# Performance work log

Hardware: AMD Instinct MI355X
Metric: run time of the kernel (lower is better)

The kernel has to match this reference:

```python
import jax, jax.numpy as jnp
import numpy as np

B, T, D = 2, 2048, 1024
H = 16
DK = D // H


def setup_inputs() -> dict:
    key = jax.random.key(0)
    ks = jax.random.split(key, 5)
    s = 1.0 / np.sqrt(D)
    return {
        "x": jax.random.normal(ks[0], (B, T, D), dtype=jnp.float32),
        "Wq": jax.random.normal(ks[1], (D, D), dtype=jnp.float32) * s,
        "bq": jnp.zeros((D,), dtype=jnp.float32),
        "Wk": jax.random.normal(ks[2], (D, D), dtype=jnp.float32) * s,
        "bk": jnp.zeros((D,), dtype=jnp.float32),
        "Wv": jax.random.normal(ks[3], (D, D), dtype=jnp.float32) * s,
        "bv": jnp.zeros((D,), dtype=jnp.float32),
        "Wo": jax.random.normal(ks[4], (D, D), dtype=jnp.float32) * s,
        "bo": jnp.zeros((D,), dtype=jnp.float32),
    }


def reference(x, Wq, bq, Wk, bk, Wv, bv, Wo, bo):
    # projections (torch Linear: x @ W.T + b; here W is stored as (in, out))
    Q = x @ Wq + bq  # (B,T,D)
    K = x @ Wk + bk
    V = x @ Wv + bv
    # split heads -> (B,H,T,dk)
    Q = Q.reshape(B, T, H, DK).transpose(0, 2, 1, 3)
    K = K.reshape(B, T, H, DK).transpose(0, 2, 1, 3)
    V = V.reshape(B, T, H, DK).transpose(0, 2, 1, 3)
    scale = 1.0 / jnp.sqrt(jnp.asarray(DK, dtype=x.dtype))
    scores = jnp.einsum("bhqd,bhkd->bhqk", Q, K) * scale  # (B,H,T,T)
    causal = jnp.tril(jnp.ones((T, T), dtype=bool))
    scores = jnp.where(causal, scores, -jnp.inf)
    weights = jax.nn.softmax(scores, axis=-1)
    # dropout is identity in eval mode
    context = jnp.einsum("bhqk,bhkd->bhqd", weights, V)
    context = context.transpose(0, 2, 1, 3).reshape(B, T, D)
    return context @ Wo + bo
```

## Files before the change

kernel.cpp:

```cpp
#include <hip/hip_runtime.h>
#include <hip/hip_bf16.h>

constexpr int Bc = 2;
constexpr int Tc = 2048;
constexpr int Mc = Bc * Tc;
constexpr float CfQ = 0.18033688011112042f;

typedef __attribute__((ext_vector_type(8))) __bf16 bf16x8;
typedef __attribute__((ext_vector_type(4))) __bf16 bf16x4;
typedef __attribute__((ext_vector_type(4))) float floatx4;

__device__ __forceinline__ void gl_lds16(const void* g, void* l) {
    __builtin_amdgcn_global_load_lds(
        (const __attribute__((address_space(1))) void*)g,
        (__attribute__((address_space(3))) void*)l, 16, 0, 0);
}

__global__ __launch_bounds__(256) void prep_all(const float* __restrict__ x,
                                                const float* __restrict__ Wq,
                                                const float* __restrict__ Wk,
                                                const float* __restrict__ Wv,
                                                const float* __restrict__ Wo,
                                                __bf16* __restrict__ xb,
                                                __bf16* __restrict__ Wqkv,
                                                __bf16* __restrict__ Wot) {
    const int z = blockIdx.z;
    const int tid = threadIdx.x;
    if (z >= 4) {
        const int lb = blockIdx.y * 16 + blockIdx.x;
        const size_t base = ((size_t)(z - 4) * 256 + lb) * 4096;
#pragma unroll
        for (int it = 0; it < 4; ++it) {
            const size_t i = base + (size_t)(it * 256 + tid) * 4;
            const float4 v = *(const float4*)(x + i);
            bf16x4 r;
            r[0] = (__bf16)v.x; r[1] = (__bf16)v.y;
            r[2] = (__bf16)v.z; r[3] = (__bf16)v.w;
            *(bf16x4*)(xb + i) = r;
        }
        return;
    }
    __shared__ float t[64][65];
    const float* W = (z == 0) ? Wq : (z == 1) ? Wk : (z == 2) ? Wv : Wo;
    __bf16* Wt = (z < 3) ? Wqkv + (size_t)z * 1024 * 1024 : Wot;
    const int k0 = blockIdx.y * 64, n0 = blockIdx.x * 64;
    const int c = tid & 63, r0 = tid >> 6;
#pragma unroll
    for (int i = 0; i < 16; ++i)
        t[r0 + i * 4][c] = W[(size_t)(k0 + r0 + i * 4) * 1024 + n0 + c];
    __syncthreads();
#pragma unroll
    for (int i = 0; i < 16; ++i) {
        const int r = r0 + i * 4;
        Wt[(size_t)(n0 + r) * 1024 + k0 + c] = (__bf16)t[c][r];
    }
}

template <int TN, bool BF16_OUT, bool FUSE_VT>
__global__ __launch_bounds__(256) void gemm_bt(const __bf16* __restrict__ A,
                                               const __bf16* __restrict__ Bt,
                                               const float* __restrict__ b0,
                                               const float* __restrict__ b1,
                                               const float* __restrict__ b2,
                                               void* __restrict__ Cv,
                                               __bf16* __restrict__ Vt,
                                               int K, int ldc) {
    constexpr int NI = TN / 32;
    __shared__ __bf16 As[128 * 64];
    __shared__ __bf16 Bs[TN * 64];
    const int tid = threadIdx.x, lane = tid & 63, wave = tid >> 6;
    const int wm = wave & 1, wn = wave >> 1;
    const int bm = blockIdx.y * 128, bn = blockIdx.x * TN;
    const __bf16* Ab = A + (size_t)bm * K;
    const __bf16* Bb = Bt + (size_t)bn * K;
    const int quad = lane >> 4, tm = lane & 15;
    const int tsw = tm & 7;

    floatx4 acc[4][NI] = {};

    for (int k0 = 0; k0 < K; k0 += 64) {
#pragma unroll
        for (int i = 0; i < 4; ++i) {
            const int s = i * 256 + tid;
            const int row = s >> 3;
            const int lc = (s & 7) ^ (row & 7);
            gl_lds16(Ab + (size_t)row * K + k0 + lc * 8, As + s * 8);
        }
#pragma unroll
        for (int i = 0; i < TN / 32; ++i) {
            const int s = i * 256 + tid;
            const int row = s >> 3;
            const int lc = (s & 7) ^ (row & 7);
            gl_lds16(Bb + (size_t)row * K + k0 + lc * 8, Bs + s * 8);
        }
        __syncthreads();
        bf16x8 af[4][2], bfv[NI][2];
#pragma unroll
        for (int mi = 0; mi < 4; ++mi) {
            const int row = (wm * 64 + mi * 16 + tm) * 64;
#pragma unroll
            for (int ks = 0; ks < 2; ++ks)
                af[mi][ks] = *(const bf16x8*)(As + row + ((ks * 4 + quad) ^ tsw) * 8);
        }
#pragma unroll
        for (int ni = 0; ni < NI; ++ni) {
            const int row = (wn * (TN / 2) + ni * 16 + tm) * 64;
#pragma unroll
            for (int ks = 0; ks < 2; ++ks)
                bfv[ni][ks] = *(const bf16x8*)(Bs + row + ((ks * 4 + quad) ^ tsw) * 8);
        }
#pragma unroll
        for (int ks = 0; ks < 2; ++ks)
#pragma unroll
            for (int mi = 0; mi < 4; ++mi)
#pragma unroll
                for (int ni = 0; ni < NI; ++ni)
                    acc[mi][ni] = __builtin_amdgcn_mfma_f32_16x16x32_bf16(
                        af[mi][ks], bfv[ni][ks], acc[mi][ni], 0, 0, 0);
        __syncthreads();
    }

#pragma unroll
    for (int ni = 0; ni < NI; ++ni) {
        const int gc = bn + wn * (TN / 2) + ni * 16 + tm;
        const float bias = (gc < 1024) ? b0[gc]
                         : (gc < 2048) ? b1[gc - 1024]
                                       : b2[gc - 2048];
        const float scale = (FUSE_VT && gc < 1024) ? CfQ : 1.0f;
#pragma unroll
        for (int mi = 0; mi < 4; ++mi) {
            const int gr0 = bm + wm * 64 + mi * 16 + quad * 4;
            if (FUSE_VT && gc >= 2048) {
                bf16x4 pv;
#pragma unroll
                for (int r = 0; r < 4; ++r) pv[r] = (__bf16)(acc[mi][ni][r] + bias);
                const int bb = gr0 >> 11, tloc = gr0 & 2047;
                const int hh = (gc - 2048) >> 6, dd = gc & 63;
                const int tperm = (tloc & ~63) + ((tloc >> 2) & 3) * 16 +
                                  ((tloc >> 4) & 3) * 4;
                *(bf16x4*)(Vt + ((size_t)(bb * 16 + hh) * 64 + dd) * 2048 + tperm) = pv;
            } else if (BF16_OUT) {
#pragma unroll
                for (int r = 0; r < 4; ++r)
                    ((__bf16*)Cv)[(size_t)(gr0 + r) * ldc + gc] =
                        (__bf16)((acc[mi][ni][r] + bias) * scale);
            } else {
#pragma unroll
                for (int r = 0; r < 4; ++r)
                    ((float*)Cv)[(size_t)(gr0 + r) * ldc + gc] =
                        acc[mi][ni][r] + bias;
            }
        }
    }
}

__global__ __launch_bounds__(512, 4) void attn_mfma(const __bf16* __restrict__ QK,
                                                    const __bf16* __restrict__ Vt,
                                                    __bf16* __restrict__ ctx) {
    constexpr float NEG = -1e30f;

    __shared__ __bf16 Ks[2][2][64 * 64];
    __shared__ __bf16 Vts[2][2][64 * 64];

    const int tid = threadIdx.x, lane = tid & 63, w = tid >> 6;
    const int g = w >> 2, wq = w & 3;
    const int c = lane & 15, quad = lane >> 4;
    const int n = blockIdx.x;
    const int bh = (n & 7) * 4 + ((n >> 3) & 3);
    const int ip = n >> 5;
    const int b = bh >> 4, h = bh & 15;

    const __bf16* Qb = QK + (size_t)(b * Tc) * 2048 + h * 64;
    const __bf16* Kb = Qb + 1024;
    const __bf16* Vtb = Vt + (size_t)bh * 64 * 2048;

    const int sw = c & 7;
    int koff0[4], koff1[4];
#pragma unroll
    for (int ni = 0; ni < 4; ++ni) {
        const int krow = ni * 16 + c;
        koff0[ni] = krow * 64 + (quad ^ sw) * 8;
        koff1[ni] = krow * 64 + ((4 + quad) ^ sw) * 8;
    }
    int voff[4][2];
#pragma unroll
    for (int di = 0; di < 4; ++di) {
        const int vrow = di * 16 + c;
#pragma unroll
        for (int pr = 0; pr < 2; ++pr)
            voff[di][pr] = vrow * 64 + ((quad * 2 + pr) ^ sw) * 8;
    }

    const int srow = tid >> 3;
    const int slc = (tid & 7) ^ (srow & 7);
    const __bf16* kgB = Kb + (size_t)srow * 2048 + slc * 8;
    const __bf16* vgB = Vtb + (size_t)srow * 2048 + slc * 8;

#pragma unroll 1
    for (int ph = 0; ph < 2; ++ph) {
        const int qt = ph ? 31 - ip : ip;
        const int nk = qt + 1;
        const int npair = (nk + 1) >> 1;

        const __bf16* qr = Qb + (size_t)(qt * 64 + wq * 16 + c) * 2048;
        const bf16x8 qf0 = *(const bf16x8*)(qr + quad * 8);
        const bf16x8 qf1 = *(const bf16x8*)(qr + 32 + quad * 8);

        floatx4 lacc = {};
        floatx4 oa[4] = {};

        auto stage = [&](int p, int sbuf) {
            const __bf16* kg = kgB + (size_t)(2 * p) * 64 * 2048;
            const __bf16* vg = vgB + 2 * p * 64;
            __bf16* kd = &Ks[sbuf][0][tid * 8];
            __bf16* vd = &Vts[sbuf][0][tid * 8];
            gl_lds16(kg, kd);
            gl_lds16(kg + (size_t)64 * 2048, kd + 4096);
            gl_lds16(vg, vd);
            gl_lds16(vg + 64, vd + 4096);
        };

        stage(0, 0);
        if (npair > 1) stage(1, 1);

        for (int kp = 0; kp < npair; ++kp) {
            const int buf = kp & 1;
            if (kp + 1 < npair) {
                asm volatile("s_waitcnt vmcnt(4)" ::: "memory");
            } else {
                asm volatile("s_waitcnt vmcnt(0)" ::: "memory");
            }
            __builtin_amdgcn_sched_barrier(0);
            __builtin_amdgcn_s_barrier();

            const int kt = 2 * kp + g;
            if (kt < nk) {
                const __bf16* ks = Ks[buf][g];
                const __bf16* vs = Vts[buf][g];

                float sv[4][4];
                __builtin_amdgcn_s_setprio(1);
#pragma unroll
                for (int ni = 0; ni < 4; ++ni) {
                    const bf16x8 kb0 = *(const bf16x8*)(ks + koff0[ni]);
                    const bf16x8 kb1 = *(const bf16x8*)(ks + koff1[ni]);
                    floatx4 a = {};
                    a = __builtin_amdgcn_mfma_f32_16x16x32_bf16(kb0, qf0, a, 0, 0, 0);
                    a = __builtin_amdgcn_mfma_f32_16x16x32_bf16(kb1, qf1, a, 0, 0, 0);
#pragma unroll
                    for (int r = 0; r < 4; ++r) sv[ni][r] = a[r];
                }
                __builtin_amdgcn_s_setprio(0);

                if (kt == qt) {
#pragma unroll
                    for (int ni = 0; ni < 4; ++ni)
#pragma unroll
                        for (int r = 0; r < 4; ++r)
                            if (ni * 16 + quad * 4 + r > wq * 16 + c) sv[ni][r] = NEG;
                }
#pragma unroll
                for (int ni = 0; ni < 4; ++ni) {
#pragma unroll
                    for (int r = 0; r < 4; ++r) sv[ni][r] = __builtin_exp2f(sv[ni][r]);
                    lacc[0] += sv[ni][0];
                    lacc[1] += sv[ni][1];
                    lacc[2] += sv[ni][2];
                    lacc[3] += sv[ni][3];
                }

                bf16x8 pb[2];
#pragma unroll
                for (int pr = 0; pr < 2; ++pr)
#pragma unroll
                    for (int j = 0; j < 4; ++j) {
                        pb[pr][j] = (__bf16)sv[pr * 2][j];
                        pb[pr][4 + j] = (__bf16)sv[pr * 2 + 1][j];
                    }

                __builtin_amdgcn_s_setprio(1);
#pragma unroll
                for (int di = 0; di < 4; ++di) {
#pragma unroll
                    for (int pr = 0; pr < 2; ++pr) {
                        const bf16x8 vf = *(const bf16x8*)(vs + voff[di][pr]);
                        oa[di] = __builtin_amdgcn_mfma_f32_16x16x32_bf16(
                            vf, pb[pr], oa[di], 0, 0, 0);
                    }
                }
                __builtin_amdgcn_s_setprio(0);
            }
            __builtin_amdgcn_sched_barrier(0);
            __builtin_amdgcn_s_barrier();
            if (kp + 2 < npair) stage(kp + 2, buf);
        }

        __syncthreads();
        float lsum = lacc[0] + lacc[1] + lacc[2] + lacc[3];
        float* sc = (float*)&Ks[0][0][0];
        if (g == 1) {
#pragma unroll
            for (int di = 0; di < 4; ++di)
                *(floatx4*)(sc + wq * 1088 + di * 256 + lane * 4) = oa[di];
            sc[wq * 1088 + 1024 + lane] = lsum;
        }
        __syncthreads();
        if (g == 0) {
#pragma unroll
            for (int di = 0; di < 4; ++di)
                oa[di] += *(const floatx4*)(sc + wq * 1088 + di * 256 + lane * 4);
            lsum += sc[wq * 1088 + 1024 + lane];
            lsum += __shfl_xor(lsum, 16);
            lsum += __shfl_xor(lsum, 32);
            const float inv = 1.f / lsum;
            __bf16* cp = ctx + (size_t)(b * Tc + qt * 64 + wq * 16 + c) * 1024 +
                         h * 64 + quad * 4;
#pragma unroll
            for (int di = 0; di < 4; ++di) {
                bf16x4 rv;
#pragma unroll
                for (int r = 0; r < 4; ++r) rv[r] = (__bf16)(oa[di][r] * inv);
                *(bf16x4*)(cp + di * 16) = rv;
            }
        }
        __syncthreads();
    }
}

extern "C" void kernel_launch(void* const* d_in, const int* in_sizes, int n_in,
                              void* d_out, int out_size, void* d_ws, size_t ws_size,
                              hipStream_t stream) {
    const float* x  = (const float*)d_in[0];
    const float* Wq = (const float*)d_in[1];
    const float* bq = (const float*)d_in[2];
    const float* Wk = (const float*)d_in[3];
    const float* bk = (const float*)d_in[4];
    const float* Wv = (const float*)d_in[5];
    const float* bv = (const float*)d_in[6];
    const float* Wo = (const float*)d_in[7];
    const float* bo = (const float*)d_in[8];

    __bf16* xb   = (__bf16*)d_ws;
    __bf16* Wqkv = xb + (size_t)Mc * 1024;
    __bf16* Wot  = Wqkv + (size_t)3072 * 1024;
    __bf16* QKb  = Wot + (size_t)1024 * 1024;
    __bf16* Vtw  = QKb + (size_t)Mc * 2048;
    __bf16* ctxb = xb;

    prep_all<<<dim3(16, 16, 8), 256, 0, stream>>>(x, Wq, Wk, Wv, Wo,
                                                  xb, Wqkv, Wot);

    gemm_bt<128, true, true><<<dim3(24, 32), 256, 0, stream>>>(
        xb, Wqkv, bq, bk, bv, QKb, Vtw, 1024, 2048);

    attn_mfma<<<dim3(512), 512, 0, stream>>>(QKb, Vtw, ctxb);

    gemm_bt<64, false, false><<<dim3(16, 32), 256, 0, stream>>>(
        ctxb, Wot, bo, bo, bo, d_out, nullptr, 1024, 1024);
}
```

Before: 179.8 us.

## Switch attention to 32x32x16 MFMA with 128-row query tiles

Rewrites the attention kernel to use 32x32x16 bf16 MFMA instead of 16x16x32. Each block now covers 128 query rows (32 per wave), so the grid halves to 256 blocks. The probability fragments are repacked through cross-lane shuffles so they can feed the PV MFMA directly, which removes the V^T time permutation in the projection GEMM epilogue. Larger tiles reuse K/V in shared memory more and issue fewer MFMA instructions, but the kernel holds more registers (launch bounds relaxed to 2 waves per SIMD) and has fewer blocks to balance the causal work.

```diff
diff --git a/kernel.cpp b/kernel.cpp
--- a/kernel.cpp
+++ b/kernel.cpp
@@ -9,11 +9,19 @@
 typedef __attribute__((ext_vector_type(8))) __bf16 bf16x8;
 typedef __attribute__((ext_vector_type(4))) __bf16 bf16x4;
 typedef __attribute__((ext_vector_type(4))) float floatx4;
+typedef __attribute__((ext_vector_type(16))) float f32x16;
+typedef __attribute__((ext_vector_type(4))) unsigned int uint4v;
 
 __device__ __forceinline__ void gl_lds16(const void* g, void* l) {
     __builtin_amdgcn_global_load_lds(
         (const __attribute__((address_space(1))) void*)g,
         (__attribute__((address_space(3))) void*)l, 16, 0, 0);
+}
+
+__device__ __forceinline__ unsigned int pkbf(float x, float y) {
+    union { __bf16 h[2]; unsigned int u; } z;
+    z.h[0] = (__bf16)x; z.h[1] = (__bf16)y;
+    return z.u;
 }
 
 __global__ __launch_bounds__(256) void prep_all(const float* __restrict__ x,
@@ -136,9 +144,7 @@
                 for (int r = 0; r < 4; ++r) pv[r] = (__bf16)(acc[mi][ni][r] + bias);
                 const int bb = gr0 >> 11, tloc = gr0 & 2047;
                 const int hh = (gc - 2048) >> 6, dd = gc & 63;
-                const int tperm = (tloc & ~63) + ((tloc >> 2) & 3) * 16 +
-                                  ((tloc >> 4) & 3) * 4;
-                *(bf16x4*)(Vt + ((size_t)(bb * 16 + hh) * 64 + dd) * 2048 + tperm) = pv;
+                *(bf16x4*)(Vt + ((size_t)(bb * 16 + hh) * 64 + dd) * 2048 + tloc) = pv;
             } else if (BF16_OUT) {
 #pragma unroll
                 for (int r = 0; r < 4; ++r)
@@ -154,7 +160,7 @@
     }
 }
 
-__global__ __launch_bounds__(512, 4) void attn_mfma(const __bf16* __restrict__ QK,
+__global__ __launch_bounds__(512, 2) void attn_mfma(const __bf16* __restrict__ QK,
                                                     const __bf16* __restrict__ Vt,
                                                     __bf16* __restrict__ ctx) {
     constexpr float NEG = -1e30f;
@@ -163,8 +169,8 @@
     __shared__ __bf16 Vts[2][2][64 * 64];
 
     const int tid = threadIdx.x, lane = tid & 63, w = tid >> 6;
-    const int g = w >> 2, wq = w & 3;
-    const int c = lane & 15, quad = lane >> 4;
+    const int g = w >> 2, ws = w & 3;
+    const int col = lane & 31, hi = lane >> 5;
     const int n = blockIdx.x;
     const int bh = (n & 7) * 4 + ((n >> 3) & 3);
     const int ip = n >> 5;
@@ -174,22 +180,13 @@
     const __bf16* Kb = Qb + 1024;
     const __bf16* Vtb = Vt + (size_t)bh * 64 * 2048;
 
-    const int sw = c & 7;
-    int koff0[4], koff1[4];
-#pragma unroll
-    for (int ni = 0; ni < 4; ++ni) {
-        const int krow = ni * 16 + c;
-        koff0[ni] = krow * 64 + (quad ^ sw) * 8;
-        koff1[ni] = krow * 64 + ((4 + quad) ^ sw) * 8;
-    }
-    int voff[4][2];
-#pragma unroll
-    for (int di = 0; di < 4; ++di) {
-        const int vrow = di * 16 + c;
-#pragma unroll
-        for (int pr = 0; pr < 2; ++pr)
-            voff[di][pr] = vrow * 64 + ((quad * 2 + pr) ^ sw) * 8;
-    }
+    const int sw = col & 7;
+    int off[2][4];
+#pragma unroll
+    for (int i = 0; i < 2; ++i)
+#pragma unroll
+        for (int cc = 0; cc < 4; ++cc)
+            off[i][cc] = (i * 32 + col) * 64 + (((cc * 2 + hi) ^ sw) * 8);
 
     const int srow = tid >> 3;
     const int slc = (tid & 7) ^ (srow & 7);
@@ -198,16 +195,18 @@
 
 #pragma unroll 1
     for (int ph = 0; ph < 2; ++ph) {
-        const int qt = ph ? 31 - ip : ip;
-        const int nk = qt + 1;
-        const int npair = (nk + 1) >> 1;
-
-        const __bf16* qr = Qb + (size_t)(qt * 64 + wq * 16 + c) * 2048;
-        const bf16x8 qf0 = *(const bf16x8*)(qr + quad * 8);
-        const bf16x8 qf1 = *(const bf16x8*)(qr + 32 + quad * 8);
+        const int qt = ph ? 15 - ip : ip;
+        const int npair = qt + 1;
+        const int qbase = qt * 128 + ws * 32;
+
+        const __bf16* qr = Qb + (size_t)(qbase + col) * 2048;
+        bf16x8 qf[4];
+#pragma unroll
+        for (int dkc = 0; dkc < 4; ++dkc)
+            qf[dkc] = *(const bf16x8*)(qr + dkc * 16 + hi * 8);
 
         floatx4 lacc = {};
-        floatx4 oa[4] = {};
+        f32x16 oa[2] = {};
 
         auto stage = [&](int p, int sbuf) {
             const __bf16* kg = kgB + (size_t)(2 * p) * 64 * 2048;
@@ -234,60 +233,67 @@
             __builtin_amdgcn_s_barrier();
 
             const int kt = 2 * kp + g;
-            if (kt < nk) {
+            const int kbase = kt * 64;
+            if (kbase <= qbase + 31) {
                 const __bf16* ks = Ks[buf][g];
                 const __bf16* vs = Vts[buf][g];
 
-                float sv[4][4];
+                f32x16 acc[2] = {};
                 __builtin_amdgcn_s_setprio(1);
 #pragma unroll
-                for (int ni = 0; ni < 4; ++ni) {
-                    const bf16x8 kb0 = *(const bf16x8*)(ks + koff0[ni]);
-                    const bf16x8 kb1 = *(const bf16x8*)(ks + koff1[ni]);
-                    floatx4 a = {};
-                    a = __builtin_amdgcn_mfma_f32_16x16x32_bf16(kb0, qf0, a, 0, 0, 0);
-                    a = __builtin_amdgcn_mfma_f32_16x16x32_bf16(kb1, qf1, a, 0, 0, 0);
-#pragma unroll
-                    for (int r = 0; r < 4; ++r) sv[ni][r] = a[r];
-                }
+                for (int kt2 = 0; kt2 < 2; ++kt2)
+#pragma unroll
+                    for (int dkc = 0; dkc < 4; ++dkc) {
+                        const bf16x8 kb = *(const bf16x8*)(ks + off[kt2][dkc]);
+                        acc[kt2] = __builtin_amdgcn_mfma_f32_32x32x16_bf16(
+                            kb, qf[dkc], acc[kt2], 0, 0, 0);
+                    }
                 __builtin_amdgcn_s_setprio(0);
 
-                if (kt == qt) {
-#pragma unroll
-                    for (int ni = 0; ni < 4; ++ni)
-#pragma unroll
-                        for (int r = 0; r < 4; ++r)
-                            if (ni * 16 + quad * 4 + r > wq * 16 + c) sv[ni][r] = NEG;
-                }
-#pragma unroll
-                for (int ni = 0; ni < 4; ++ni) {
-#pragma unroll
-                    for (int r = 0; r < 4; ++r) sv[ni][r] = __builtin_exp2f(sv[ni][r]);
-                    lacc[0] += sv[ni][0];
-                    lacc[1] += sv[ni][1];
-                    lacc[2] += sv[ni][2];
-                    lacc[3] += sv[ni][3];
-                }
-
-                bf16x8 pb[2];
-#pragma unroll
-                for (int pr = 0; pr < 2; ++pr)
-#pragma unroll
-                    for (int j = 0; j < 4; ++j) {
-                        pb[pr][j] = (__bf16)sv[pr * 2][j];
-                        pb[pr][4 + j] = (__bf16)sv[pr * 2 + 1][j];
+                if (kp == npair - 1) {
+#pragma unroll
+                    for (int kt2 = 0; kt2 < 2; ++kt2)
+#pragma unroll
+                        for (int reg = 0; reg < 16; ++reg) {
+                            const int kloc = kt2 * 32 + (reg & 3) + 8 * (reg >> 2) + 4 * hi;
+                            if (kbase + kloc > qbase + col) acc[kt2][reg] = NEG;
+                        }
+                }
+#pragma unroll
+                for (int kt2 = 0; kt2 < 2; ++kt2)
+#pragma unroll
+                    for (int reg = 0; reg < 16; ++reg) {
+                        const float p = __builtin_exp2f(acc[kt2][reg]);
+                        acc[kt2][reg] = p;
+                        lacc[reg & 3] += p;
                     }
 
+                bf16x8 pf[4];
+#pragma unroll
+                for (int tc = 0; tc < 4; ++tc) {
+                    const int kt2 = tc >> 1, c16 = (tc & 1) * 8;
+                    const unsigned int a0 = pkbf(acc[kt2][c16 + 0], acc[kt2][c16 + 1]);
+                    const unsigned int a1 = pkbf(acc[kt2][c16 + 2], acc[kt2][c16 + 3]);
+                    const unsigned int b0 = pkbf(acc[kt2][c16 + 4], acc[kt2][c16 + 5]);
+                    const unsigned int b1 = pkbf(acc[kt2][c16 + 6], acc[kt2][c16 + 7]);
+                    const unsigned int s0 = hi ? a0 : b0, s1 = hi ? a1 : b1;
+                    const unsigned int r0 = __shfl_xor(s0, 32);
+                    const unsigned int r1 = __shfl_xor(s1, 32);
+                    uint4v dv;
+                    dv[0] = hi ? r0 : a0; dv[1] = hi ? r1 : a1;
+                    dv[2] = hi ? b0 : r0; dv[3] = hi ? b1 : r1;
+                    pf[tc] = __builtin_bit_cast(bf16x8, dv);
+                }
+
                 __builtin_amdgcn_s_setprio(1);
 #pragma unroll
-                for (int di = 0; di < 4; ++di) {
-#pragma unroll
-                    for (int pr = 0; pr < 2; ++pr) {
-                        const bf16x8 vf = *(const bf16x8*)(vs + voff[di][pr]);
-                        oa[di] = __builtin_amdgcn_mfma_f32_16x16x32_bf16(
-                            vf, pb[pr], oa[di], 0, 0, 0);
+                for (int dt = 0; dt < 2; ++dt)
+#pragma unroll
+                    for (int tc = 0; tc < 4; ++tc) {
+                        const bf16x8 vf = *(const bf16x8*)(vs + off[dt][tc]);
+                        oa[dt] = __builtin_amdgcn_mfma_f32_32x32x16_bf16(
+                            vf, pf[tc], oa[dt], 0, 0, 0);
                     }
-                }
                 __builtin_amdgcn_s_setprio(0);
             }
             __builtin_amdgcn_sched_barrier(0);
@@ -296,32 +302,46 @@
         }
 
         __syncthreads();
-        float lsum = lacc[0] + lacc[1] + lacc[2] + lacc[3];
-        float* sc = (float*)&Ks[0][0][0];
+        float lt = lacc[0] + lacc[1] + lacc[2] + lacc[3];
+        lt += __shfl_xor(lt, 32);
+        float* sco = (float*)&Ks[0][0][0];
+        float* scl = (float*)&Vts[0][0][0];
         if (g == 1) {
 #pragma unroll
-            for (int di = 0; di < 4; ++di)
-                *(floatx4*)(sc + wq * 1088 + di * 256 + lane * 4) = oa[di];
-            sc[wq * 1088 + 1024 + lane] = lsum;
+            for (int dt = 0; dt < 2; ++dt)
+#pragma unroll
+                for (int a = 0; a < 4; ++a) {
+                    floatx4 t4;
+                    t4[0] = oa[dt][4 * a + 0]; t4[1] = oa[dt][4 * a + 1];
+                    t4[2] = oa[dt][4 * a + 2]; t4[3] = oa[dt][4 * a + 3];
+                    *(floatx4*)(sco + (dt * 4 + a) * 1024 + ws * 256 + lane * 4) = t4;
+                }
+            scl[ws * 64 + lane] = lt;
         }
         __syncthreads();
         if (g == 0) {
 #pragma unroll
-            for (int di = 0; di < 4; ++di)
-                oa[di] += *(const floatx4*)(sc + wq * 1088 + di * 256 + lane * 4);
-            lsum += sc[wq * 1088 + 1024 + lane];
-            lsum += __shfl_xor(lsum, 16);
-            lsum += __shfl_xor(lsum, 32);
-            const float inv = 1.f / lsum;
-            __bf16* cp = ctx + (size_t)(b * Tc + qt * 64 + wq * 16 + c) * 1024 +
-                         h * 64 + quad * 4;
-#pragma unroll
-            for (int di = 0; di < 4; ++di) {
-                bf16x4 rv;
-#pragma unroll
-                for (int r = 0; r < 4; ++r) rv[r] = (__bf16)(oa[di][r] * inv);
-                *(bf16x4*)(cp + di * 16) = rv;
-            }
+            for (int dt = 0; dt < 2; ++dt)
+#pragma unroll
+                for (int a = 0; a < 4; ++a) {
+                    const floatx4 t4 =
+                        *(const floatx4*)(sco + (dt * 4 + a) * 1024 + ws * 256 + lane * 4);
+                    oa[dt][4 * a + 0] += t4[0]; oa[dt][4 * a + 1] += t4[1];
+                    oa[dt][4 * a + 2] += t4[2]; oa[dt][4 * a + 3] += t4[3];
+                }
+            lt += scl[ws * 64 + lane];
+            const float inv = 1.f / lt;
+            __bf16* cp = ctx + (size_t)(b * Tc + qbase + col) * 1024 + h * 64 + hi * 4;
+#pragma unroll
+            for (int dt = 0; dt < 2; ++dt)
+#pragma unroll
+                for (int a = 0; a < 4; ++a) {
+                    bf16x4 rv;
+#pragma unroll
+                    for (int r = 0; r < 4; ++r)
+                        rv[r] = (__bf16)(oa[dt][4 * a + r] * inv);
+                    *(bf16x4*)(cp + dt * 32 + a * 8) = rv;
+                }
         }
         __syncthreads();
     }
@@ -353,7 +373,7 @@
     gemm_bt<128, true, true><<<dim3(24, 32), 256, 0, stream>>>(
         xb, Wqkv, bq, bk, bv, QKb, Vtw, 1024, 2048);
 
-    attn_mfma<<<dim3(512), 512, 0, stream>>>(QKb, Vtw, ctxb);
+    attn_mfma<<<dim3(256), 512, 0, stream>>>(QKb, Vtw, ctxb);
 
     gemm_bt<64, false, false><<<dim3(16, 32), 256, 0, stream>>>(
         ctxb, Wot, bo, bo, bo, d_out, nullptr, 1024, 1024);
```

New measurement: 193.1 us. 7.4% more time.

## Double-buffer GEMM LDS tiles with K=32 steps and async prefetch

Applied to the files above, without the earlier changes.

Restructures the bf16 GEMM main loop into a two-stage software pipeline. K-step shrinks from 64 to 32, LDS tiles are double-buffered, and direct global-to-LDS loads for step k+2 are issued while step k computes. Manual vmcnt waits and s_setprio around the MFMA block replace the per-iteration load/sync/compute serialization, with the XOR swizzle adjusted for 32-wide rows. The risks are that hand-counted vmcnt values are fragile, and that the smaller K-step means twice as many barriers.

```diff
diff --git a/kernel.cpp b/kernel.cpp
--- a/kernel.cpp
+++ b/kernel.cpp
@@ -66,58 +66,73 @@
                                                __bf16* __restrict__ Vt,
                                                int K, int ldc) {
     constexpr int NI = TN / 32;
-    __shared__ __bf16 As[128 * 64];
-    __shared__ __bf16 Bs[TN * 64];
+    constexpr int NB = TN / 64;
+    __shared__ __bf16 As[2][128 * 32];
+    __shared__ __bf16 Bs[2][TN * 32];
     const int tid = threadIdx.x, lane = tid & 63, wave = tid >> 6;
     const int wm = wave & 1, wn = wave >> 1;
     const int bm = blockIdx.y * 128, bn = blockIdx.x * TN;
     const __bf16* Ab = A + (size_t)bm * K;
     const __bf16* Bb = Bt + (size_t)bn * K;
     const int quad = lane >> 4, tm = lane & 15;
-    const int tsw = tm & 7;
+    const int xsw = (tm >> 1) & 3;
 
     floatx4 acc[4][NI] = {};
 
-    for (int k0 = 0; k0 < K; k0 += 64) {
-#pragma unroll
-        for (int i = 0; i < 4; ++i) {
+    auto stage = [&](int k0, int sbuf) {
+#pragma unroll
+        for (int i = 0; i < 2; ++i) {
             const int s = i * 256 + tid;
-            const int row = s >> 3;
-            const int lc = (s & 7) ^ (row & 7);
-            gl_lds16(Ab + (size_t)row * K + k0 + lc * 8, As + s * 8);
-        }
-#pragma unroll
-        for (int i = 0; i < TN / 32; ++i) {
+            const int row = s >> 2;
+            const int lc = (s & 3) ^ ((row >> 1) & 3);
+            gl_lds16(Ab + (size_t)row * K + k0 + lc * 8, &As[sbuf][s * 8]);
+        }
+#pragma unroll
+        for (int i = 0; i < NB; ++i) {
             const int s = i * 256 + tid;
-            const int row = s >> 3;
-            const int lc = (s & 7) ^ (row & 7);
-            gl_lds16(Bb + (size_t)row * K + k0 + lc * 8, Bs + s * 8);
-        }
-        __syncthreads();
-        bf16x8 af[4][2], bfv[NI][2];
-#pragma unroll
-        for (int mi = 0; mi < 4; ++mi) {
-            const int row = (wm * 64 + mi * 16 + tm) * 64;
-#pragma unroll
-            for (int ks = 0; ks < 2; ++ks)
-                af[mi][ks] = *(const bf16x8*)(As + row + ((ks * 4 + quad) ^ tsw) * 8);
-        }
-#pragma unroll
-        for (int ni = 0; ni < NI; ++ni) {
-            const int row = (wn * (TN / 2) + ni * 16 + tm) * 64;
-#pragma unroll
-            for (int ks = 0; ks < 2; ++ks)
-                bfv[ni][ks] = *(const bf16x8*)(Bs + row + ((ks * 4 + quad) ^ tsw) * 8);
-        }
-#pragma unroll
-        for (int ks = 0; ks < 2; ++ks)
-#pragma unroll
-            for (int mi = 0; mi < 4; ++mi)
-#pragma unroll
-                for (int ni = 0; ni < NI; ++ni)
-                    acc[mi][ni] = __builtin_amdgcn_mfma_f32_16x16x32_bf16(
-                        af[mi][ks], bfv[ni][ks], acc[mi][ni], 0, 0, 0);
-        __syncthreads();
+            const int row = s >> 2;
+            const int lc = (s & 3) ^ ((row >> 1) & 3);
+            gl_lds16(Bb + (size_t)row * K + k0 + lc * 8, &Bs[sbuf][s * 8]);
+        }
+    };
+
+    const int nstep = K >> 5;
+    stage(0, 0);
+    stage(32, 1);
+
+    for (int ks = 0; ks < nstep; ++ks) {
+        const int buf = ks & 1;
+        if (ks + 1 < nstep) {
+            if constexpr (TN == 128)
+                asm volatile("s_waitcnt vmcnt(4)" ::: "memory");
+            else
+                asm volatile("s_waitcnt vmcnt(3)" ::: "memory");
+        } else {
+            asm volatile("s_waitcnt vmcnt(0)" ::: "memory");
+        }
+        __builtin_amdgcn_sched_barrier(0);
+        __builtin_amdgcn_s_barrier();
+
+        bf16x8 af[4], bfv[NI];
+#pragma unroll
+        for (int mi = 0; mi < 4; ++mi)
+            af[mi] = *(const bf16x8*)(&As[buf][(wm * 64 + mi * 16 + tm) * 32 +
+                                               ((quad ^ xsw) * 8)]);
+#pragma unroll
+        for (int ni = 0; ni < NI; ++ni)
+            bfv[ni] = *(const bf16x8*)(&Bs[buf][(wn * (TN / 2) + ni * 16 + tm) * 32 +
+                                                ((quad ^ xsw) * 8)]);
+        __builtin_amdgcn_s_setprio(1);
+#pragma unroll
+        for (int mi = 0; mi < 4; ++mi)
+#pragma unroll
+            for (int ni = 0; ni < NI; ++ni)
+                acc[mi][ni] = __builtin_amdgcn_mfma_f32_16x16x32_bf16(
+                    af[mi], bfv[ni], acc[mi][ni], 0, 0, 0);
+        __builtin_amdgcn_s_setprio(0);
+        __builtin_amdgcn_sched_barrier(0);
+        __builtin_amdgcn_s_barrier();
+        if (ks + 2 < nstep) stage((ks + 2) * 32, buf);
     }
 
 #pragma unroll
```

Measured after the change: 179.2 us. Within noise of the previous version (-0.3%).
